# Kernel optimization log

Measured on AMD Instinct MI355X. Metric: run time of the kernel, lower is better.

Reference implementation:

```python
import jax, jax.numpy as jnp
import numpy as np

N, E, IN, H, C = 50000, 800000, 256, 4, 64  # nodes, edges, input_dim, heads, hidden_dim


def setup_inputs() -> dict:
    key = jax.random.key(0)
    ks = jax.random.split(key, 12)
    rn = lambda k, shp, s: jax.random.normal(k, shp, jnp.float32) * s
    glorot = lambda fi, fo: (2.0 / (fi + fo)) ** 0.5
    return {
        "x": rn(ks[0], (N, IN), 1.0),
        "edge_index": jax.random.randint(ks[1], (2, E), 0, N, dtype=jnp.int32),
        # gat1: in=IN, out=H*C, concat=True
        "W1": rn(ks[2], (IN, H * C), glorot(IN, H * C)),
        "att_src1": rn(ks[3], (H, C), 0.1),
        "att_dst1": rn(ks[4], (H, C), 0.1),
        "b1": jnp.zeros((H * C,), jnp.float32),
        # gat2: in=H*C, out=C, heads=1, concat=False
        "W2": rn(ks[5], (H * C, C), glorot(H * C, C)),
        "att_src2": rn(ks[6], (1, C), 0.1),
        "att_dst2": rn(ks[7], (1, C), 0.1),
        "b2": jnp.zeros((C,), jnp.float32),
        # attention pooling head + entity scorer
        "att_w": rn(ks[8], (C, 1), 0.1),
        "att_b": jnp.zeros((1,), jnp.float32),
        "fc_w": rn(ks[9], (C, 1), 0.1),
        "fc_b": jnp.zeros((1,), jnp.float32),
    }


def _gat_conv(x, src, dst, W, a_src, a_dst, bias, concat):
    """PyG GATConv (self-loops already appended to src/dst)."""
    n = x.shape[0]
    heads, ch = a_src.shape
    h = (x @ W).reshape(n, heads, ch)                      # [N,H,C]
    s = jnp.sum(h * a_src[None], axis=-1)                  # [N,H]
    d = jnp.sum(h * a_dst[None], axis=-1)                  # [N,H]
    e = jax.nn.leaky_relu(s[src] + d[dst], 0.2)            # [Etot,H]
    # segment softmax over incoming edges of each dst node
    m = jax.ops.segment_max(e, dst, num_segments=n)        # [N,H]
    m = jnp.where(jnp.isfinite(m), m, 0.0)
    ex = jnp.exp(e - m[dst])
    den = jax.ops.segment_sum(ex, dst, num_segments=n)
    alpha = ex / den[dst]                                  # [Etot,H]
    out = jax.ops.segment_sum(h[src] * alpha[:, :, None], dst, num_segments=n)  # [N,H,C]
    out = out.reshape(n, heads * ch) if concat else out.mean(axis=1)
    return out + bias


def reference(x, edge_index, W1, att_src1, att_dst1, b1, W2, att_src2, att_dst2, b2,
              att_w, att_b, fc_w, fc_b):
    n = x.shape[0]
    loop = jnp.arange(n, dtype=edge_index.dtype)           # add_self_loops=True
    src = jnp.concatenate([edge_index[0], loop])
    dst = jnp.concatenate([edge_index[1], loop])
    h = jax.nn.relu(_gat_conv(x, src, dst, W1, att_src1, att_dst1, b1, True))   # [N,H*C]
    h = jax.nn.relu(_gat_conv(h, src, dst, W2, att_src2, att_dst2, b2, False))  # [N,C]
    aw = jax.nn.softmax(h @ att_w + att_b, axis=0)         # softmax over all nodes, [N,1]
    global_rep = jnp.sum(aw * h, axis=0)                   # [C]
    entity_probs = jax.nn.sigmoid(h @ fc_w + fc_b).squeeze(-1)  # [N]
    return entity_probs, global_rep
```

## Files before the change

kernel.cpp:

```cpp
#include <hip/hip_runtime.h>
#include <hip/hip_bf16.h>
#include <math.h>

#define N_NODES 50000
#define N_EDGES 800000
#define ETOT    850000
#define IN_DIM  256
#define HC      256
#define HEADS   4
#define CD      64

typedef _Float16  f16x8 __attribute__((ext_vector_type(8)));
typedef _Float16  f16x4 __attribute__((ext_vector_type(4)));
typedef float     f32x4 __attribute__((ext_vector_type(4)));

static __device__ __forceinline__ float lrelu(float x) { return x > 0.f ? x : 0.2f * x; }

__global__ void k_init(int* counts, int* cursor) {
    int i = blockIdx.x * 256 + threadIdx.x;
    if (i < N_NODES) { counts[i] = 1; cursor[i] = 0; }
}

__global__ void k_degree(const int* __restrict__ dst, int* __restrict__ counts) {
    int i = blockIdx.x * 256 + threadIdx.x;
    if (i < N_EDGES) atomicAdd(&counts[dst[i]], 1);
}

__global__ __launch_bounds__(1024) void k_scan_a(const int* __restrict__ counts,
                                                 int* __restrict__ rowptr,
                                                 int* __restrict__ bsum) {
    __shared__ int sd[1024];
    int t = threadIdx.x;
    int i = blockIdx.x * 1024 + t;
    int v = (i < N_NODES) ? counts[i] : 0;
    sd[t] = v; __syncthreads();
    for (int off = 1; off < 1024; off <<= 1) {
        int add = (t >= off) ? sd[t - off] : 0;
        __syncthreads();
        sd[t] += add;
        __syncthreads();
    }
    if (i < N_NODES) rowptr[i + 1] = sd[t];
    if (t == 1023) bsum[blockIdx.x] = sd[1023];
    if (i == 0) rowptr[0] = 0;
}

__global__ void k_scan_b(int* bsum, int nb) {
    if (threadIdx.x == 0) {
        int run = 0;
        for (int b = 0; b < nb; ++b) { int t = bsum[b]; bsum[b] = run; run += t; }
    }
}

__global__ void k_scan_c(int* __restrict__ rowptr, const int* __restrict__ bsum) {
    int i = blockIdx.x * 256 + threadIdx.x;
    if (i < N_NODES) rowptr[i + 1] += bsum[i >> 10];
}

__global__ void k_scatter(const int* __restrict__ src, const int* __restrict__ dst,
                          const int* __restrict__ rowptr, int* __restrict__ cursor,
                          int* __restrict__ src_sorted) {
    int i = blockIdx.x * 256 + threadIdx.x;
    if (i >= ETOT) return;
    int s, d;
    if (i < N_EDGES) { s = src[i]; d = dst[i]; }
    else             { s = i - N_EDGES; d = s; }
    int pos = rowptr[d] + atomicAdd(&cursor[d], 1);
    src_sorted[pos] = s;
}

__global__ void k_convx16(const float* __restrict__ x, _Float16* __restrict__ o) {
    int i = blockIdx.x * 256 + threadIdx.x;
    if (i >= N_NODES * IN_DIM / 4) return;
    float4 v = reinterpret_cast<const float4*>(x)[i];
    f16x4 h = {(_Float16)v.x, (_Float16)v.y, (_Float16)v.z, (_Float16)v.w};
    reinterpret_cast<f16x4*>(o)[i] = h;
}

__global__ void k_convw16(const float* __restrict__ W, _Float16* __restrict__ oT, int Nc) {
    int idx = blockIdx.x * 256 + threadIdx.x;
    if (idx >= Nc * 256) return;
    int n = idx >> 8, k = idx & 255;
    oT[idx] = (_Float16)W[(size_t)k * Nc + n];
}

__global__ __launch_bounds__(256) void k_gemm_h(
    const _Float16* __restrict__ A, const _Float16* __restrict__ BT,
    _Float16* __restrict__ O,
    float* __restrict__ s_out, float* __restrict__ d_out,
    const float* __restrict__ a_s, const float* __restrict__ a_d,
    int M, int Nc)
{
    const int lane = threadIdx.x & 63, w = threadIdx.x >> 6;
    const int row0 = blockIdx.y * 256 + w * 64;
    const int col0 = blockIdx.x * 64;
    const int hs = Nc >> 6;
    const int rl = lane & 15, kg = lane >> 4;

    f32x4 acc[4][4];
    const f32x4 fzero = {0.f, 0.f, 0.f, 0.f};
    #pragma unroll
    for (int m = 0; m < 4; ++m)
        #pragma unroll
        for (int n = 0; n < 4; ++n) acc[m][n] = fzero;

    size_t aoff[4], boff[4];
    #pragma unroll
    for (int m = 0; m < 4; ++m) {
        int r = row0 + m * 16 + rl; if (r >= M) r = M - 1;
        aoff[m] = (size_t)r * 256 + kg * 8;
    }
    #pragma unroll
    for (int n = 0; n < 4; ++n) {
        int c = col0 + n * 16 + rl;
        boff[n] = (size_t)c * 256 + kg * 8;
    }

    #pragma unroll 2
    for (int k0 = 0; k0 < 256; k0 += 32) {
        f16x8 a_[4], b_[4];
        #pragma unroll
        for (int m = 0; m < 4; ++m)
            a_[m] = *reinterpret_cast<const f16x8*>(A + aoff[m] + k0);
        #pragma unroll
        for (int n = 0; n < 4; ++n)
            b_[n] = *reinterpret_cast<const f16x8*>(BT + boff[n] + k0);
        #pragma unroll
        for (int m = 0; m < 4; ++m)
            #pragma unroll
            for (int n = 0; n < 4; ++n)
                acc[m][n] = __builtin_amdgcn_mfma_f32_16x16x32_f16(a_[m], b_[n], acc[m][n], 0, 0, 0);
    }

    float as_[4], ad_[4];
    #pragma unroll
    for (int n = 0; n < 4; ++n) {
        as_[n] = a_s[col0 + n * 16 + rl];
        ad_[n] = a_d[col0 + n * 16 + rl];
    }
    #pragma unroll
    for (int m = 0; m < 4; ++m) {
        #pragma unroll
        for (int r = 0; r < 4; ++r) {
            int row = row0 + m * 16 + kg * 4 + r;
            float v0 = acc[m][0][r], v1 = acc[m][1][r], v2 = acc[m][2][r], v3 = acc[m][3][r];
            float sp = v0 * as_[0] + v1 * as_[1] + v2 * as_[2] + v3 * as_[3];
            float dp = v0 * ad_[0] + v1 * ad_[1] + v2 * ad_[2] + v3 * ad_[3];
            #pragma unroll
            for (int off = 1; off < 16; off <<= 1) {
                sp += __shfl_xor(sp, off, 64);
                dp += __shfl_xor(dp, off, 64);
            }
            if (row < M) {
                _Float16* o = O + (size_t)row * Nc + col0 + rl;
                o[0]  = (_Float16)v0;
                o[16] = (_Float16)v1;
                o[32] = (_Float16)v2;
                o[48] = (_Float16)v3;
                if (rl == 0) {
                    s_out[(size_t)row * hs + blockIdx.x] = sp;
                    d_out[(size_t)row * hs + blockIdx.x] = dp;
                }
            }
        }
    }
}

__global__ __launch_bounds__(256) void k_agg1(const int* __restrict__ rowptr,
                                              const int* __restrict__ srcs,
                                              const _Float16* __restrict__ h1f,
                                              const float* __restrict__ s1,
                                              const float* __restrict__ d1,
                                              const float* __restrict__ b1,
                                              _Float16* __restrict__ o_f16) {
    const int w = threadIdx.x >> 6, l = threadIdx.x & 63;
    const int v = blockIdx.x * 4 + w;
    if (v >= N_NODES) return;
    __shared__ float exs[4][64][4];
    __shared__ int   us[4][64];
    const int row0 = rowptr[v], row1 = rowptr[v + 1];
    const float4 dv = *reinterpret_cast<const float4*>(d1 + 4 * v);
    const int head = l >> 4;
    float a0 = 0.f, a1 = 0.f, a2 = 0.f, a3 = 0.f, den = 0.f;

    for (int c0 = row0; c0 < row1; c0 += 64) {
        const int nc = min(64, row1 - c0);
        if (l < nc) {
            int u = srcs[c0 + l];
            float4 s = *reinterpret_cast<const float4*>(s1 + 4 * u);
            us[w][l] = u;
            exs[w][l][0] = __expf(lrelu(s.x + dv.x));
            exs[w][l][1] = __expf(lrelu(s.y + dv.y));
            exs[w][l][2] = __expf(lrelu(s.z + dv.z));
            exs[w][l][3] = __expf(lrelu(s.w + dv.w));
        }
        __builtin_amdgcn_wave_barrier();
        for (int j = 0; j < nc; ++j) {
            int u = us[w][j];
            float ex = exs[w][j][head];
            f16x4 hv = *reinterpret_cast<const f16x4*>(h1f + (size_t)u * 256 + l * 4);
            a0 += ex * (float)hv[0];
            a1 += ex * (float)hv[1];
            a2 += ex * (float)hv[2];
            a3 += ex * (float)hv[3];
            den += ex;
        }
        __builtin_amdgcn_wave_barrier();
    }
    const float4 bb = *reinterpret_cast<const float4*>(b1 + l * 4);
    f16x4 o4;
    o4[0] = (_Float16)fmaxf(a0 / den + bb.x, 0.f);
    o4[1] = (_Float16)fmaxf(a1 / den + bb.y, 0.f);
    o4[2] = (_Float16)fmaxf(a2 / den + bb.z, 0.f);
    o4[3] = (_Float16)fmaxf(a3 / den + bb.w, 0.f);
    *reinterpret_cast<f16x4*>(o_f16 + (size_t)v * 256 + l * 4) = o4;
}

__global__ __launch_bounds__(256) void k_agg2(const int* __restrict__ rowptr,
                                              const int* __restrict__ srcs,
                                              const _Float16* __restrict__ t2f,
                                              const float* __restrict__ s2,
                                              const float* __restrict__ d2,
                                              const float* __restrict__ b2,
                                              float* __restrict__ h2) {
    const int w = threadIdx.x >> 6, l = threadIdx.x & 63;
    const int v = blockIdx.x * 4 + w;
    if (v >= N_NODES) return;
    __shared__ float exw[4][64];
    __shared__ int   uw[4][64];
    const int row0 = rowptr[v], row1 = rowptr[v + 1];
    const float dvv = d2[v];
    float acc = 0.f, den = 0.f;
    for (int c0 = row0; c0 < row1; c0 += 64) {
        int nc = min(64, row1 - c0);
        if (l < nc) {
            int u = srcs[c0 + l];
            uw[w][l] = u;
            exw[w][l] = __expf(lrelu(s2[u] + dvv));
        }
        __builtin_amdgcn_wave_barrier();
        for (int j = 0; j < nc; ++j) {
            int u = uw[w][j];
            float ex = exw[w][j];
            acc += ex * (float)t2f[(size_t)u * CD + l];
            den += ex;
        }
        __builtin_amdgcn_wave_barrier();
    }
    h2[(size_t)v * CD + l] = fmaxf(acc / den + b2[l], 0.f);
}

__global__ __launch_bounds__(256) void k_head(const float* __restrict__ h2,
                                              const float* __restrict__ att_w,
                                              const float* __restrict__ att_b,
                                              const float* __restrict__ fc_w,
                                              const float* __restrict__ fc_b,
                                              float* __restrict__ logit,
                                              float* __restrict__ outp) {
    int wave = threadIdx.x >> 6, lane = threadIdx.x & 63;
    int v = blockIdx.x * 4 + wave;
    if (v >= N_NODES) return;
    float hv = h2[(size_t)v * CD + lane];
    float a = hv * att_w[lane];
    float f = hv * fc_w[lane];
    #pragma unroll
    for (int off = 32; off; off >>= 1) {
        a += __shfl_down(a, off, 64);
        f += __shfl_down(f, off, 64);
    }
    if (lane == 0) {
        logit[v] = a + att_b[0];
        float z = f + fc_b[0];
        outp[v] = 1.f / (1.f + __expf(-z));
    }
}

__global__ __launch_bounds__(256) void k_pmax(const float* __restrict__ logit,
                                              float* __restrict__ pmax) {
    __shared__ float sd[256];
    int t = threadIdx.x;
    float lm = -1e30f;
    for (int i = blockIdx.x * 256 + t; i < N_NODES; i += gridDim.x * 256)
        lm = fmaxf(lm, logit[i]);
    sd[t] = lm; __syncthreads();
    for (int s = 128; s; s >>= 1) { if (t < s) sd[t] = fmaxf(sd[t], sd[t + s]); __syncthreads(); }
    if (t == 0) pmax[blockIdx.x] = sd[0];
}

__global__ __launch_bounds__(256) void k_finmax(const float* __restrict__ pmax,
                                                float* __restrict__ gmax,
                                                float* __restrict__ gsum,
                                                float* __restrict__ gvec) {
    __shared__ float sd[256];
    int t = threadIdx.x;
    sd[t] = pmax[t];
    __syncthreads();
    for (int s = 128; s; s >>= 1) { if (t < s) sd[t] = fmaxf(sd[t], sd[t + s]); __syncthreads(); }
    if (t == 0) { *gmax = sd[0]; *gsum = 0.f; }
    if (t < 64) gvec[t] = 0.f;
}

__global__ __launch_bounds__(256) void k_pool(const float* __restrict__ h2,
                                              const float* __restrict__ logit,
                                              const float* __restrict__ gmax,
                                              float* __restrict__ gsum,
                                              float* __restrict__ gvec) {
    int wave = threadIdx.x >> 6, lane = threadIdx.x & 63;
    __shared__ float acc_s[4][64];
    __shared__ float ws_s[4];
    float m = *gmax;
    float acc = 0.f, wsum = 0.f;
    int gw = blockIdx.x * 4 + wave;
    int nw = gridDim.x * 4;
    for (int v = gw; v < N_NODES; v += nw) {
        float w = __expf(logit[v] - m);
        acc += w * h2[(size_t)v * CD + lane];
        if (lane == 0) wsum += w;
    }
    acc_s[wave][lane] = acc;
    if (lane == 0) ws_s[wave] = wsum;
    __syncthreads();
    if (threadIdx.x < 64) {
        float a = acc_s[0][threadIdx.x] + acc_s[1][threadIdx.x] +
                  acc_s[2][threadIdx.x] + acc_s[3][threadIdx.x];
        atomicAdd(&gvec[threadIdx.x], a);
    }
    if (threadIdx.x == 0)
        atomicAdd(gsum, ws_s[0] + ws_s[1] + ws_s[2] + ws_s[3]);
}

__global__ void k_writeout(const float* __restrict__ gvec,
                           const float* __restrict__ gsum,
                           float* __restrict__ outg) {
    int t = threadIdx.x;
    if (t < 64) outg[t] = gvec[t] / *gsum;
}

extern "C" void kernel_launch(void* const* d_in, const int* in_sizes, int n_in,
                              void* d_out, int out_size, void* d_ws, size_t ws_size,
                              hipStream_t stream) {
    const float* x    = (const float*)d_in[0];
    const int*   ei   = (const int*)d_in[1];
    const float* W1   = (const float*)d_in[2];
    const float* as1  = (const float*)d_in[3];
    const float* ad1  = (const float*)d_in[4];
    const float* b1   = (const float*)d_in[5];
    const float* W2   = (const float*)d_in[6];
    const float* as2  = (const float*)d_in[7];
    const float* ad2  = (const float*)d_in[8];
    const float* b2   = (const float*)d_in[9];
    const float* attw = (const float*)d_in[10];
    const float* attb = (const float*)d_in[11];
    const float* fcw  = (const float*)d_in[12];
    const float* fcb  = (const float*)d_in[13];
    const int* srcE = ei;
    const int* dstE = ei + N_EDGES;

    char* ws = (char*)d_ws;
    size_t off = 0;
    auto take = [&](size_t bytes) -> void* {
        void* p = ws + off;
        off += (bytes + 255) & ~(size_t)255;
        return p;
    };
    _Float16* h1f  = (_Float16*)take((size_t)N_NODES * HC * 2);
    _Float16* t2f  = (_Float16*)take((size_t)N_NODES * CD * 2);
    float* h2   = (float*)take((size_t)N_NODES * CD * 4);
    float* s1   = (float*)take((size_t)N_NODES * 4 * 4);
    float* d1   = (float*)take((size_t)N_NODES * 4 * 4);
    float* s2   = (float*)take((size_t)N_NODES * 4);
    float* d2   = (float*)take((size_t)N_NODES * 4);
    int* counts = (int*)take((size_t)N_NODES * 4);
    int* cursor = (int*)take((size_t)N_NODES * 4);
    int* rowptr = (int*)take((size_t)(N_NODES + 1) * 4);
    int* bsum   = (int*)take(64 * 4);
    int* src_sorted = (int*)take((size_t)ETOT * 4);
    _Float16* xf16 = (_Float16*)take((size_t)N_NODES * IN_DIM * 2);
    _Float16* W1T  = (_Float16*)take(256 * 256 * 2);
    _Float16* W2T  = (_Float16*)take(64 * 256 * 2);
    float* logit = (float*)take((size_t)N_NODES * 4);
    float* pmax  = (float*)take(256 * 4);
    float* gmax  = (float*)take(4);
    float* gsum  = (float*)take(4);
    float* gvec  = (float*)take(64 * 4);
    _Float16* out1f = xf16;

    k_init<<<(N_NODES + 255) / 256, 256, 0, stream>>>(counts, cursor);
    k_degree<<<(N_EDGES + 255) / 256, 256, 0, stream>>>(dstE, counts);
    int nb = (N_NODES + 1023) / 1024;
    k_scan_a<<<nb, 1024, 0, stream>>>(counts, rowptr, bsum);
    k_scan_b<<<1, 64, 0, stream>>>(bsum, nb);
    k_scan_c<<<(N_NODES + 255) / 256, 256, 0, stream>>>(rowptr, bsum);
    k_scatter<<<(ETOT + 255) / 256, 256, 0, stream>>>(srcE, dstE, rowptr, cursor, src_sorted);

    k_convx16<<<(N_NODES * IN_DIM / 4 + 255) / 256, 256, 0, stream>>>(x, xf16);
    k_convw16<<<(256 * 256 + 255) / 256, 256, 0, stream>>>(W1, W1T, HC);
    k_convw16<<<(64 * 256 + 255) / 256, 256, 0, stream>>>(W2, W2T, CD);

    k_gemm_h<<<dim3(HC / 64, (N_NODES + 255) / 256), 256, 0, stream>>>(
        xf16, W1T, h1f, s1, d1, as1, ad1, N_NODES, HC);
    k_agg1<<<(N_NODES + 3) / 4, 256, 0, stream>>>(rowptr, src_sorted, h1f, s1, d1, b1, out1f);

    k_gemm_h<<<dim3(CD / 64, (N_NODES + 255) / 256), 256, 0, stream>>>(
        out1f, W2T, t2f, s2, d2, as2, ad2, N_NODES, CD);
    k_agg2<<<(N_NODES + 3) / 4, 256, 0, stream>>>(rowptr, src_sorted, t2f, s2, d2, b2, h2);

    k_head<<<(N_NODES + 3) / 4, 256, 0, stream>>>(h2, attw, attb, fcw, fcb, logit, (float*)d_out);
    k_pmax<<<256, 256, 0, stream>>>(logit, pmax);
    k_finmax<<<1, 256, 0, stream>>>(pmax, gmax, gsum, gvec);
    k_pool<<<256, 256, 0, stream>>>(h2, logit, gmax, gsum, gvec);
    k_writeout<<<1, 64, 0, stream>>>(gvec, gsum, (float*)d_out + N_NODES);
}
```

Baseline: 386.6 us.

## Process two edges per wave with wider loads in GAT aggregation; fuse head into agg2

In both aggregation kernels each half of the wave now handles a different edge, so every lane loads 8 fp16 (agg1) or 2 fp16 (agg2) per edge. Partial sums are combined with an xor-32 shuffle, and padded edge slots get zero weight. The scorer/attention-logit head is fused into agg2, removing one kernel launch and a full read of h2. The aim is fewer loop iterations and more in-flight memory requests on these latency-bound gather loops, at the cost of extra shuffles and more accumulator registers.

```diff
diff --git a/kernel.cpp b/kernel.cpp
--- a/kernel.cpp
+++ b/kernel.cpp
@@ -12,6 +12,7 @@
 
 typedef _Float16  f16x8 __attribute__((ext_vector_type(8)));
 typedef _Float16  f16x4 __attribute__((ext_vector_type(4)));
+typedef _Float16  f16x2 __attribute__((ext_vector_type(2)));
 typedef float     f32x4 __attribute__((ext_vector_type(4)));
 
 static __device__ __forceinline__ float lrelu(float x) { return x > 0.f ? x : 0.2f * x; }
@@ -180,40 +181,62 @@
     __shared__ int   us[4][64];
     const int row0 = rowptr[v], row1 = rowptr[v + 1];
     const float4 dv = *reinterpret_cast<const float4*>(d1 + 4 * v);
-    const int head = l >> 4;
-    float a0 = 0.f, a1 = 0.f, a2 = 0.f, a3 = 0.f, den = 0.f;
+    const int cl = l & 31, hf = l >> 5;
+    const int head = cl >> 3;
+    float a0=0.f,a1=0.f,a2=0.f,a3=0.f,a4=0.f,a5=0.f,a6=0.f,a7=0.f;
+    float den = 0.f;
 
     for (int c0 = row0; c0 < row1; c0 += 64) {
         const int nc = min(64, row1 - c0);
-        if (l < nc) {
-            int u = srcs[c0 + l];
-            float4 s = *reinterpret_cast<const float4*>(s1 + 4 * u);
+        {
+            int idx = (l < nc) ? c0 + l : row0;
+            int u = srcs[idx];
             us[w][l] = u;
-            exs[w][l][0] = __expf(lrelu(s.x + dv.x));
-            exs[w][l][1] = __expf(lrelu(s.y + dv.y));
-            exs[w][l][2] = __expf(lrelu(s.z + dv.z));
-            exs[w][l][3] = __expf(lrelu(s.w + dv.w));
+            if (l < nc) {
+                float4 s = *reinterpret_cast<const float4*>(s1 + 4 * u);
+                exs[w][l][0] = __expf(lrelu(s.x + dv.x));
+                exs[w][l][1] = __expf(lrelu(s.y + dv.y));
+                exs[w][l][2] = __expf(lrelu(s.z + dv.z));
+                exs[w][l][3] = __expf(lrelu(s.w + dv.w));
+            } else {
+                exs[w][l][0] = 0.f; exs[w][l][1] = 0.f;
+                exs[w][l][2] = 0.f; exs[w][l][3] = 0.f;
+            }
         }
         __builtin_amdgcn_wave_barrier();
-        for (int j = 0; j < nc; ++j) {
-            int u = us[w][j];
-            float ex = exs[w][j][head];
-            f16x4 hv = *reinterpret_cast<const f16x4*>(h1f + (size_t)u * 256 + l * 4);
-            a0 += ex * (float)hv[0];
-            a1 += ex * (float)hv[1];
-            a2 += ex * (float)hv[2];
-            a3 += ex * (float)hv[3];
+        const int jEnd = (nc + 1) & ~1;
+        for (int j = 0; j < jEnd; j += 2) {
+            int jj = j + hf;
+            int u = us[w][jj];
+            float ex = exs[w][jj][head];
+            f16x8 hv = *reinterpret_cast<const f16x8*>(h1f + (size_t)u * 256 + cl * 8);
+            a0 += ex * (float)hv[0]; a1 += ex * (float)hv[1];
+            a2 += ex * (float)hv[2]; a3 += ex * (float)hv[3];
+            a4 += ex * (float)hv[4]; a5 += ex * (float)hv[5];
+            a6 += ex * (float)hv[6]; a7 += ex * (float)hv[7];
             den += ex;
         }
         __builtin_amdgcn_wave_barrier();
     }
-    const float4 bb = *reinterpret_cast<const float4*>(b1 + l * 4);
-    f16x4 o4;
-    o4[0] = (_Float16)fmaxf(a0 / den + bb.x, 0.f);
-    o4[1] = (_Float16)fmaxf(a1 / den + bb.y, 0.f);
-    o4[2] = (_Float16)fmaxf(a2 / den + bb.z, 0.f);
-    o4[3] = (_Float16)fmaxf(a3 / den + bb.w, 0.f);
-    *reinterpret_cast<f16x4*>(o_f16 + (size_t)v * 256 + l * 4) = o4;
+    a0 += __shfl_xor(a0, 32, 64); a1 += __shfl_xor(a1, 32, 64);
+    a2 += __shfl_xor(a2, 32, 64); a3 += __shfl_xor(a3, 32, 64);
+    a4 += __shfl_xor(a4, 32, 64); a5 += __shfl_xor(a5, 32, 64);
+    a6 += __shfl_xor(a6, 32, 64); a7 += __shfl_xor(a7, 32, 64);
+    den += __shfl_xor(den, 32, 64);
+    if (hf == 0) {
+        const float4 bb0 = *reinterpret_cast<const float4*>(b1 + cl * 8);
+        const float4 bb1 = *reinterpret_cast<const float4*>(b1 + cl * 8 + 4);
+        f16x8 o8;
+        o8[0] = (_Float16)fmaxf(a0 / den + bb0.x, 0.f);
+        o8[1] = (_Float16)fmaxf(a1 / den + bb0.y, 0.f);
+        o8[2] = (_Float16)fmaxf(a2 / den + bb0.z, 0.f);
+        o8[3] = (_Float16)fmaxf(a3 / den + bb0.w, 0.f);
+        o8[4] = (_Float16)fmaxf(a4 / den + bb1.x, 0.f);
+        o8[5] = (_Float16)fmaxf(a5 / den + bb1.y, 0.f);
+        o8[6] = (_Float16)fmaxf(a6 / den + bb1.z, 0.f);
+        o8[7] = (_Float16)fmaxf(a7 / den + bb1.w, 0.f);
+        *reinterpret_cast<f16x8*>(o_f16 + (size_t)v * 256 + cl * 8) = o8;
+    }
 }
 
 __global__ __launch_bounds__(256) void k_agg2(const int* __restrict__ rowptr,
@@ -222,7 +245,13 @@
                                               const float* __restrict__ s2,
                                               const float* __restrict__ d2,
                                               const float* __restrict__ b2,
-                                              float* __restrict__ h2) {
+                                              const float* __restrict__ att_w,
+                                              const float* __restrict__ att_b,
+                                              const float* __restrict__ fc_w,
+                                              const float* __restrict__ fc_b,
+                                              float* __restrict__ h2,
+                                              float* __restrict__ logit,
+                                              float* __restrict__ outp) {
     const int w = threadIdx.x >> 6, l = threadIdx.x & 63;
     const int v = blockIdx.x * 4 + w;
     if (v >= N_NODES) return;
@@ -230,48 +259,48 @@
     __shared__ int   uw[4][64];
     const int row0 = rowptr[v], row1 = rowptr[v + 1];
     const float dvv = d2[v];
-    float acc = 0.f, den = 0.f;
+    const int cl = l & 31, hf = l >> 5;
+    float c0a = 0.f, c1a = 0.f, den = 0.f;
     for (int c0 = row0; c0 < row1; c0 += 64) {
         int nc = min(64, row1 - c0);
-        if (l < nc) {
-            int u = srcs[c0 + l];
+        {
+            int idx = (l < nc) ? c0 + l : row0;
+            int u = srcs[idx];
             uw[w][l] = u;
-            exw[w][l] = __expf(lrelu(s2[u] + dvv));
+            exw[w][l] = (l < nc) ? __expf(lrelu(s2[u] + dvv)) : 0.f;
         }
         __builtin_amdgcn_wave_barrier();
-        for (int j = 0; j < nc; ++j) {
-            int u = uw[w][j];
-            float ex = exw[w][j];
-            acc += ex * (float)t2f[(size_t)u * CD + l];
+        const int jEnd = (nc + 1) & ~1;
+        for (int j = 0; j < jEnd; j += 2) {
+            int jj = j + hf;
+            int u = uw[w][jj];
+            float ex = exw[w][jj];
+            f16x2 hv = *reinterpret_cast<const f16x2*>(t2f + (size_t)u * CD + cl * 2);
+            c0a += ex * (float)hv[0];
+            c1a += ex * (float)hv[1];
             den += ex;
         }
         __builtin_amdgcn_wave_barrier();
     }
-    h2[(size_t)v * CD + l] = fmaxf(acc / den + b2[l], 0.f);
-}
-
-__global__ __launch_bounds__(256) void k_head(const float* __restrict__ h2,
-                                              const float* __restrict__ att_w,
-                                              const float* __restrict__ att_b,
-                                              const float* __restrict__ fc_w,
-                                              const float* __restrict__ fc_b,
-                                              float* __restrict__ logit,
-                                              float* __restrict__ outp) {
-    int wave = threadIdx.x >> 6, lane = threadIdx.x & 63;
-    int v = blockIdx.x * 4 + wave;
-    if (v >= N_NODES) return;
-    float hv = h2[(size_t)v * CD + lane];
-    float a = hv * att_w[lane];
-    float f = hv * fc_w[lane];
-    #pragma unroll
-    for (int off = 32; off; off >>= 1) {
-        a += __shfl_down(a, off, 64);
-        f += __shfl_down(f, off, 64);
-    }
-    if (lane == 0) {
-        logit[v] = a + att_b[0];
-        float z = f + fc_b[0];
-        outp[v] = 1.f / (1.f + __expf(-z));
+    c0a += __shfl_xor(c0a, 32, 64);
+    c1a += __shfl_xor(c1a, 32, 64);
+    den += __shfl_xor(den, 32, 64);
+    float h0 = fmaxf(c0a / den + b2[cl * 2], 0.f);
+    float h1 = fmaxf(c1a / den + b2[cl * 2 + 1], 0.f);
+    float a = h0 * att_w[cl * 2] + h1 * att_w[cl * 2 + 1];
+    float f = h0 * fc_w[cl * 2]  + h1 * fc_w[cl * 2 + 1];
+    #pragma unroll
+    for (int off = 1; off < 32; off <<= 1) {
+        a += __shfl_xor(a, off, 64);
+        f += __shfl_xor(f, off, 64);
+    }
+    if (hf == 0) {
+        float2 hv2 = {h0, h1};
+        *reinterpret_cast<float2*>(h2 + (size_t)v * CD + cl * 2) = hv2;
+        if (cl == 0) {
+            logit[v] = a + att_b[0];
+            outp[v] = 1.f / (1.f + __expf(-(f + fc_b[0])));
+        }
     }
 }
 
@@ -403,9 +432,9 @@
 
     k_gemm_h<<<dim3(CD / 64, (N_NODES + 255) / 256), 256, 0, stream>>>(
         out1f, W2T, t2f, s2, d2, as2, ad2, N_NODES, CD);
-    k_agg2<<<(N_NODES + 3) / 4, 256, 0, stream>>>(rowptr, src_sorted, t2f, s2, d2, b2, h2);
-
-    k_head<<<(N_NODES + 3) / 4, 256, 0, stream>>>(h2, attw, attb, fcw, fcb, logit, (float*)d_out);
+    k_agg2<<<(N_NODES + 3) / 4, 256, 0, stream>>>(rowptr, src_sorted, t2f, s2, d2, b2,
+                                                  attw, attb, fcw, fcb, h2, logit, (float*)d_out);
+
     k_pmax<<<256, 256, 0, stream>>>(logit, pmax);
     k_finmax<<<1, 256, 0, stream>>>(pmax, gmax, gsum, gvec);
     k_pool<<<256, 256, 0, stream>>>(h2, logit, gmax, gsum, gvec);
```

Measured after the change: 389.4 us. No clear change (+0.7%).
